# Kernel optimization log

Hardware: AMD Instinct MI355X
Metric: run time of the kernel (lower is better)

Reference implementation:

```python
import jax, jax.numpy as jnp
import numpy as np

B, F, T, EPT, S, E, H, LVL = 16384, 512, 4, 2, 2, 256, 128, 2

def _ple_level(xs_task, x_sh, w_task, b_task, w_sh, b_sh, w_gate, b_gate, w_gsh=None, b_gsh=None):
    # xs_task: [T,B,I] per-task inputs; x_sh: [B,I] shared input
    task_out = jax.nn.relu(jnp.einsum('tbi,teio->tbeo', xs_task, w_task) + b_task[:, None])  # [T,B,EPT,E]
    sh_out = jax.nn.relu(jnp.einsum('bi,sio->bso', x_sh, w_sh) + b_sh)                       # [B,S,E]
    t = task_out.shape[0]
    experts = jnp.concatenate([task_out, jnp.broadcast_to(sh_out[None], (t,) + sh_out.shape)], axis=2)  # [T,B,EPT+S,E]
    gate = jax.nn.softmax(jnp.einsum('tbi,tig->tbg', xs_task, w_gate) + b_gate[:, None], axis=-1)
    task_next = jnp.einsum('tbg,tbge->tbe', gate, experts)  # [T,B,E]
    sh_next = None
    if w_gsh is not None:
        # all experts ordered task0_exp0, task0_exp1, task1_exp0, ..., then shared
        bsz = x_sh.shape[0]
        all_exp = jnp.concatenate([jnp.transpose(task_out, (1, 0, 2, 3)).reshape(bsz, -1, task_out.shape[-1]), sh_out], axis=1)
        gsh = jax.nn.softmax(x_sh @ w_gsh + b_gsh, axis=-1)
        sh_next = jnp.einsum('bg,bge->be', gsh, all_exp)
    return task_next, sh_next

def setup_inputs() -> dict:
    key = jax.random.key(0)
    ks = jax.random.split(key, 16)
    sc = 0.02
    d = {
        'x': jax.random.normal(ks[0], (B, F), jnp.float32),
        # level 0 (in_dim=F, has shared gate)
        'w_task0': jax.random.normal(ks[1], (T, EPT, F, E), jnp.float32) * sc,
        'b_task0': jnp.zeros((T, EPT, E), jnp.float32),
        'w_sh0': jax.random.normal(ks[2], (S, F, E), jnp.float32) * sc,
        'b_sh0': jnp.zeros((S, E), jnp.float32),
        'w_gate0': jax.random.normal(ks[3], (T, F, EPT + S), jnp.float32) * sc,
        'b_gate0': jnp.zeros((T, EPT + S), jnp.float32),
        'w_gsh0': jax.random.normal(ks[4], (F, T * EPT + S), jnp.float32) * sc,
        'b_gsh0': jnp.zeros((T * EPT + S,), jnp.float32),
        # level 1 (last; in_dim=E, no shared gate)
        'w_task1': jax.random.normal(ks[5], (T, EPT, E, E), jnp.float32) * sc,
        'b_task1': jnp.zeros((T, EPT, E), jnp.float32),
        'w_sh1': jax.random.normal(ks[6], (S, E, E), jnp.float32) * sc,
        'b_sh1': jnp.zeros((S, E), jnp.float32),
        'w_gate1': jax.random.normal(ks[7], (T, E, EPT + S), jnp.float32) * sc,
        'b_gate1': jnp.zeros((T, EPT + S), jnp.float32),
        # towers
        'w_tw': jax.random.normal(ks[8], (T, E, H), jnp.float32) * sc,
        'b_tw': jnp.zeros((T, H), jnp.float32),
        'w_out': jax.random.normal(ks[9], (T, H, 2), jnp.float32) * sc,
        'b_out': jnp.zeros((T, 2), jnp.float32),
    }
    return d

def reference(x, w_task0, b_task0, w_sh0, b_sh0, w_gate0, b_gate0, w_gsh0, b_gsh0,
              w_task1, b_task1, w_sh1, b_sh1, w_gate1, b_gate1,
              w_tw, b_tw, w_out, b_out):
    xs_task = jnp.broadcast_to(x[None], (T,) + x.shape)  # all tasks see same input at level 0
    t1, sh1 = _ple_level(xs_task, x, w_task0, b_task0, w_sh0, b_sh0, w_gate0, b_gate0, w_gsh0, b_gsh0)
    t2, _ = _ple_level(t1, sh1, w_task1, b_task1, w_sh1, b_sh1, w_gate1, b_gate1)
    h = jax.nn.relu(jnp.einsum('tbe,teh->tbh', t2, w_tw) + b_tw[:, None])
    logits = jnp.einsum('tbh,tho->tbo', h, w_out) + b_out[:, None]
    p = jax.nn.softmax(logits, axis=-1)
    return jnp.clip(p, 1e-15, 1.0 - 1e-15)  # [T,B,2]
```

## Files before the change

### kernel.cpp

```cpp
#include <hip/hip_runtime.h>

typedef unsigned short u16;
typedef __bf16 bf16x8 __attribute__((ext_vector_type(8)));
typedef float f32x4 __attribute__((ext_vector_type(4)));
typedef u16 u16x8 __attribute__((ext_vector_type(8)));

#define B_ 16384

__device__ __forceinline__ u16 f2b(float f){
  unsigned u = __builtin_bit_cast(unsigned, f);
  u = (u + 0x7FFFu + ((u >> 16) & 1u)) >> 16;
  return (u16)u;
}
__device__ __forceinline__ float b2f(u16 v){
  return __builtin_bit_cast(float, ((unsigned)v) << 16);
}
__device__ __forceinline__ void ld8(const u16* __restrict__ p, float* f){
  u16x8 v = *(const u16x8*)p;
  #pragma unroll
  for (int j = 0; j < 8; ++j) f[j] = b2f(v[j]);
}
__device__ __forceinline__ void st8(u16* __restrict__ p, const float* f){
  u16x8 v;
  #pragma unroll
  for (int j = 0; j < 8; ++j) v[j] = f2b(f[j]);
  *(u16x8*)p = v;
}

__device__ __forceinline__ void gload16(const u16* g, u16* lds){
  __builtin_amdgcn_global_load_lds(
      (const __attribute__((address_space(1))) unsigned int*)g,
      (__attribute__((address_space(3))) unsigned int*)lds, 16, 0, 0);
}

__device__ __forceinline__ void gemm_core(const u16* __restrict__ A,
                                          const u16* __restrict__ Wt,
                                          int K, int m0, int n0,
                                          u16* sA, u16* sB,
                                          f32x4 acc[4][4])
{
  const int tid  = threadIdx.x;
  const int lane = tid & 63;
  const int wave = tid >> 6;
  const int wm   = ((tid >> 7) & 1) * 64;
  const int wn   = ((tid >> 6) & 1) * 64;

  f32x4 zero = {0.f, 0.f, 0.f, 0.f};
  #pragma unroll
  for (int mi = 0; mi < 4; ++mi)
    #pragma unroll
    for (int ni = 0; ni < 4; ++ni)
      acc[mi][ni] = zero;

  const int srow  = lane >> 3;
  const int gslot = (lane & 7) ^ srow;

  const int nsteps = K >> 6;
  for (int ks = 0; ks < nsteps; ++ks) {
    const u16* aB = A  + (size_t)(m0 + wave * 32 + srow) * K + ks * 64 + gslot * 8;
    const u16* bB = Wt + (size_t)(n0 + wave * 32 + srow) * K + ks * 64 + gslot * 8;
    u16* lA = sA + (wave * 4) * 512;
    u16* lB = sB + (wave * 4) * 512;
    #pragma unroll
    for (int i = 0; i < 4; ++i) {
      gload16(aB + (size_t)i * 8 * K, lA + i * 512);
      gload16(bB + (size_t)i * 8 * K, lB + i * 512);
    }
    __syncthreads();
    #pragma unroll
    for (int kk = 0; kk < 2; ++kk) {
      bf16x8 av[4], bv[4];
      #pragma unroll
      for (int mi = 0; mi < 4; ++mi) {
        int r = wm + mi * 16 + (lane & 15);
        int slot = kk * 4 + (lane >> 4);
        av[mi] = *(const bf16x8*)(sA + r * 64 + ((slot ^ (r & 7)) << 3));
      }
      #pragma unroll
      for (int ni = 0; ni < 4; ++ni) {
        int r = wn + ni * 16 + (lane & 15);
        int slot = kk * 4 + (lane >> 4);
        bv[ni] = *(const bf16x8*)(sB + r * 64 + ((slot ^ (r & 7)) << 3));
      }
      #pragma unroll
      for (int mi = 0; mi < 4; ++mi)
        #pragma unroll
        for (int ni = 0; ni < 4; ++ni)
          acc[mi][ni] = __builtin_amdgcn_mfma_f32_16x16x32_bf16(av[mi], bv[ni], acc[mi][ni], 0, 0, 0);
    }
    __syncthreads();
  }
}


__global__ __launch_bounds__(256) void k_gemm0(const u16* __restrict__ xb,
    const u16* __restrict__ Wt0, const float* __restrict__ bias0,
    u16* __restrict__ E0, float* __restrict__ G0L)
{
  __shared__ __align__(16) u16 sm[2 * 128 * 64];
  f32x4 acc[4][4];
  const int bid = blockIdx.x;
  const int swz = (bid & 7) * 336 + (bid >> 3);
  const int m0 = (swz / 21) * 128, n0 = (swz % 21) * 128;
  gemm_core(xb, Wt0, 512, m0, n0, sm, sm + 8192, acc);
  const int lane = threadIdx.x & 63;
  const int wm = ((threadIdx.x >> 7) & 1) * 64, wn = ((threadIdx.x >> 6) & 1) * 64;
  #pragma unroll
  for (int mi = 0; mi < 4; ++mi)
    #pragma unroll
    for (int ni = 0; ni < 4; ++ni) {
      int gcol = n0 + wn + ni * 16 + (lane & 15);
      float bias = bias0[gcol];
      #pragma unroll
      for (int r = 0; r < 4; ++r) {
        int grow = m0 + wm + mi * 16 + ((lane >> 4) << 2) + r;
        float v = acc[mi][ni][r] + bias;
        if (gcol < 2560)      E0[(size_t)grow * 2560 + gcol] = f2b(fmaxf(v, 0.f));
        else if (gcol < 2586) G0L[(size_t)grow * 26 + (gcol - 2560)] = v;
      }
    }
}

__global__ __launch_bounds__(256) void k_mix0(const u16* __restrict__ E0,
    const float* __restrict__ G0L, u16* __restrict__ T1SH)
{
  const int b = blockIdx.x * 8 + (threadIdx.x >> 5);
  const int e0 = (threadIdx.x & 31) * 8;
  const float* gl = G0L + (size_t)b * 26;
  float g[4][4];
  #pragma unroll
  for (int t = 0; t < 4; ++t) {
    float l0 = gl[t*4+0], l1 = gl[t*4+1], l2 = gl[t*4+2], l3 = gl[t*4+3];
    float m = fmaxf(fmaxf(l0, l1), fmaxf(l2, l3));
    float e0e = expf(l0-m), e1 = expf(l1-m), e2 = expf(l2-m), e3 = expf(l3-m);
    float inv = 1.f / (e0e + e1 + e2 + e3);
    g[t][0] = e0e*inv; g[t][1] = e1*inv; g[t][2] = e2*inv; g[t][3] = e3*inv;
  }
  float gs[10];
  {
    float m = gl[16];
    #pragma unroll
    for (int j = 1; j < 10; ++j) m = fmaxf(m, gl[16 + j]);
    float s = 0.f;
    #pragma unroll
    for (int j = 0; j < 10; ++j) { gs[j] = expf(gl[16 + j] - m); s += gs[j]; }
    float inv = 1.f / s;
    #pragma unroll
    for (int j = 0; j < 10; ++j) gs[j] *= inv;
  }
  const u16* row = E0 + (size_t)b * 2560;
  float sh0[8], sh1[8], shacc[8];
  ld8(row + 2048 + e0, sh0);
  ld8(row + 2304 + e0, sh1);
  #pragma unroll
  for (int j = 0; j < 8; ++j) shacc[j] = gs[8]*sh0[j] + gs[9]*sh1[j];
  #pragma unroll
  for (int t = 0; t < 4; ++t) {
    float te0[8], te1[8], v[8];
    ld8(row + (t*2+0)*256 + e0, te0);
    ld8(row + (t*2+1)*256 + e0, te1);
    #pragma unroll
    for (int j = 0; j < 8; ++j) {
      v[j] = g[t][0]*te0[j] + g[t][1]*te1[j] + g[t][2]*sh0[j] + g[t][3]*sh1[j];
      shacc[j] += gs[t*2+0]*te0[j] + gs[t*2+1]*te1[j];
    }
    st8(T1SH + ((size_t)t * B_ + b) * 256 + e0, v);
  }
  st8(T1SH + ((size_t)4 * B_ + b) * 256 + e0, shacc);
}

__global__ __launch_bounds__(256) void k_gemm1(const u16* __restrict__ T1SH,
    const u16* __restrict__ Wt1, const float* __restrict__ bias1,
    u16* __restrict__ E1, float* __restrict__ G1L, u16* __restrict__ SH1E)
{
  const int z = blockIdx.z;
  const int m0 = blockIdx.x * 128, n0 = blockIdx.y * 128;
  if (z == 4 && n0 >= 512) return;
  __shared__ __align__(16) u16 sm[2 * 128 * 64];
  f32x4 acc[4][4];
  gemm_core(T1SH + (size_t)z * B_ * 256, Wt1 + (size_t)z * 640 * 256, 256, m0, n0, sm, sm + 8192, acc);
  const int lane = threadIdx.x & 63;
  const int wm = ((threadIdx.x >> 7) & 1) * 64, wn = ((threadIdx.x >> 6) & 1) * 64;
  const float* bias = bias1 + z * 640;
  #pragma unroll
  for (int mi = 0; mi < 4; ++mi)
    #pragma unroll
    for (int ni = 0; ni < 4; ++ni) {
      int gcol = n0 + wn + ni * 16 + (lane & 15);
      float bv = bias[gcol];
      #pragma unroll
      for (int r = 0; r < 4; ++r) {
        int grow = m0 + wm + mi * 16 + ((lane >> 4) << 2) + r;
        float v = acc[mi][ni][r] + bv;
        if (z < 4) {
          if (gcol < 512)      E1[((size_t)z * B_ + grow) * 512 + gcol] = f2b(fmaxf(v, 0.f));
          else if (gcol < 516) G1L[((size_t)z * B_ + grow) * 4 + (gcol - 512)] = v;
        } else {
          if (gcol < 512)      SH1E[(size_t)grow * 512 + gcol] = f2b(fmaxf(v, 0.f));
        }
      }
    }
}

__global__ __launch_bounds__(256) void k_mix1(const u16* __restrict__ E1,
    const float* __restrict__ G1L, const u16* __restrict__ SH1E, u16* __restrict__ T2)
{
  const int b = blockIdx.x * 8 + (threadIdx.x >> 5);
  const int e0 = (threadIdx.x & 31) * 8;
  float sh0[8], sh1[8];
  ld8(SH1E + (size_t)b * 512 + e0, sh0);
  ld8(SH1E + (size_t)b * 512 + 256 + e0, sh1);
  #pragma unroll
  for (int t = 0; t < 4; ++t) {
    const float* gl = G1L + ((size_t)t * B_ + b) * 4;
    float l0 = gl[0], l1 = gl[1], l2 = gl[2], l3 = gl[3];
    float m = fmaxf(fmaxf(l0, l1), fmaxf(l2, l3));
    float x0 = expf(l0-m), x1 = expf(l1-m), x2 = expf(l2-m), x3 = expf(l3-m);
    float inv = 1.f / (x0 + x1 + x2 + x3);
    float g0 = x0*inv, g1 = x1*inv, g2 = x2*inv, g3 = x3*inv;
    float te0[8], te1[8], v[8];
    ld8(E1 + ((size_t)t * B_ + b) * 512 + e0, te0);
    ld8(E1 + ((size_t)t * B_ + b) * 512 + 256 + e0, te1);
    #pragma unroll
    for (int j = 0; j < 8; ++j)
      v[j] = g0*te0[j] + g1*te1[j] + g2*sh0[j] + g3*sh1[j];
    st8(T2 + ((size_t)t * B_ + b) * 256 + e0, v);
  }
}

__global__ __launch_bounds__(256) void k_tower(const u16* __restrict__ T2,
    const u16* __restrict__ Wtw, const float* __restrict__ b_tw,
    const float* __restrict__ w_out, const float* __restrict__ b_out,
    float* __restrict__ out)
{
  __shared__ __align__(16) u16 sm[2 * 128 * 64];
  __shared__ float part[2][128][2];
  f32x4 acc[4][4];
  const int z = blockIdx.z;
  const int m0 = blockIdx.x * 128;
  gemm_core(T2 + (size_t)z * B_ * 256, Wtw + (size_t)z * 128 * 256, 256, m0, 0, sm, sm + 8192, acc);
  const int lane = threadIdx.x & 63;
  const int wm = ((threadIdx.x >> 7) & 1) * 64, wn = ((threadIdx.x >> 6) & 1) * 64;
  #pragma unroll
  for (int mi = 0; mi < 4; ++mi) {
    #pragma unroll
    for (int r = 0; r < 4; ++r) {
      float p0 = 0.f, p1 = 0.f;
      #pragma unroll
      for (int ni = 0; ni < 4; ++ni) {
        int col = wn + ni * 16 + (lane & 15);
        float h = fmaxf(acc[mi][ni][r] + b_tw[z * 128 + col], 0.f);
        p0 += h * w_out[(z * 128 + col) * 2 + 0];
        p1 += h * w_out[(z * 128 + col) * 2 + 1];
      }
      #pragma unroll
      for (int off = 1; off < 16; off <<= 1) {
        p0 += __shfl_xor(p0, off);
        p1 += __shfl_xor(p1, off);
      }
      if ((lane & 15) == 0) {
        int rowl = wm + mi * 16 + ((lane >> 4) << 2) + r;
        part[wn >> 6][rowl][0] = p0;
        part[wn >> 6][rowl][1] = p1;
      }
    }
  }
  __syncthreads();
  if (threadIdx.x < 128) {
    int rowl = threadIdx.x;
    float l0 = part[0][rowl][0] + part[1][rowl][0] + b_out[z * 2 + 0];
    float l1 = part[0][rowl][1] + part[1][rowl][1] + b_out[z * 2 + 1];
    float mx = fmaxf(l0, l1);
    float e0 = expf(l0 - mx), e1 = expf(l1 - mx);
    float inv = 1.f / (e0 + e1);
    float p0 = fminf(fmaxf(e0 * inv, 1e-15f), 1.0f);
    float p1 = fminf(fmaxf(e1 * inv, 1e-15f), 1.0f);
    size_t o = ((size_t)z * B_ + m0 + rowl) * 2;
    out[o] = p0; out[o + 1] = p1;
  }
}

__global__ void k_prep(const float* __restrict__ x,
    const float* __restrict__ w_task0, const float* __restrict__ b_task0,
    const float* __restrict__ w_sh0,   const float* __restrict__ b_sh0,
    const float* __restrict__ w_gate0, const float* __restrict__ b_gate0,
    const float* __restrict__ w_gsh0,  const float* __restrict__ b_gsh0,
    const float* __restrict__ w_task1, const float* __restrict__ b_task1,
    const float* __restrict__ w_sh1,   const float* __restrict__ b_sh1,
    const float* __restrict__ w_gate1, const float* __restrict__ b_gate1,
    const float* __restrict__ w_tw,
    u16* __restrict__ xb, u16* __restrict__ Wt0, float* __restrict__ bias0,
    u16* __restrict__ Wt1, float* __restrict__ bias1, u16* __restrict__ Wtw)
{
  size_t i = (size_t)blockIdx.x * 256 + threadIdx.x;
  const size_t S_X8  = (size_t)16384 * 512 / 8;
  const size_t S_WT0 = (size_t)2688 * 512;
  const size_t S_B0  = 2688;
  const size_t S_WT1 = (size_t)5 * 640 * 256;
  const size_t S_B1  = 5 * 640;
  const size_t S_WTW = (size_t)4 * 128 * 256;

  if (i < S_X8) {
    size_t o = i * 8;
    float4 a = *(const float4*)(x + o);
    float4 b = *(const float4*)(x + o + 4);
    u16x8 v;
    v[0] = f2b(a.x); v[1] = f2b(a.y); v[2] = f2b(a.z); v[3] = f2b(a.w);
    v[4] = f2b(b.x); v[5] = f2b(b.y); v[6] = f2b(b.z); v[7] = f2b(b.w);
    *(u16x8*)(xb + o) = v;
    return;
  }
  i -= S_X8;
  if (i < S_WT0) {
    int c = (int)(i / 512), f = (int)(i % 512);
    float v = 0.f;
    if (c < 2048)      { int te = c >> 8, o = c & 255; v = w_task0[((size_t)te * 512 + f) * 256 + o]; }
    else if (c < 2560) { int s = (c - 2048) >> 8, o = c & 255; v = w_sh0[((size_t)s * 512 + f) * 256 + o]; }
    else if (c < 2576) { int q = c - 2560; int t = q >> 2, gg = q & 3; v = w_gate0[((size_t)t * 512 + f) * 4 + gg]; }
    else if (c < 2586) { int j = c - 2576; v = w_gsh0[(size_t)f * 10 + j]; }
    Wt0[i] = f2b(v);
    return;
  }
  i -= S_WT0;
  if (i < S_B0) {
    int c = (int)i; float v = 0.f;
    if (c < 2048)      { int te = c >> 8, o = c & 255; v = b_task0[te * 256 + o]; }
    else if (c < 2560) { int s = (c - 2048) >> 8, o = c & 255; v = b_sh0[s * 256 + o]; }
    else if (c < 2576) { v = b_gate0[c - 2560]; }
    else if (c < 2586) { v = b_gsh0[c - 2576]; }
    bias0[c] = v;
    return;
  }
  i -= S_B0;
  if (i < S_WT1) {
    int z = (int)(i / (640 * 256)); int rem = (int)(i % (640 * 256));
    int c = rem / 256, f = rem % 256;
    float v = 0.f;
    if (z < 4) {
      if (c < 512)      { int ee = c >> 8, o = c & 255; v = w_task1[(((size_t)(z * 2 + ee)) * 256 + f) * 256 + o]; }
      else if (c < 516) { int gg = c - 512; v = w_gate1[((size_t)z * 256 + f) * 4 + gg]; }
    } else {
      if (c < 512)      { int s = c >> 8, o = c & 255; v = w_sh1[((size_t)s * 256 + f) * 256 + o]; }
    }
    Wt1[i] = f2b(v);
    return;
  }
  i -= S_WT1;
  if (i < S_B1) {
    int z = (int)(i / 640); int c = (int)(i % 640);
    float v = 0.f;
    if (z < 4) {
      if (c < 512)      { int ee = c >> 8, o = c & 255; v = b_task1[(z * 2 + ee) * 256 + o]; }
      else if (c < 516) { v = b_gate1[z * 4 + (c - 512)]; }
    } else {
      if (c < 512)      { int s = c >> 8, o = c & 255; v = b_sh1[s * 256 + o]; }
    }
    bias1[(size_t)z * 640 + c] = v;
    return;
  }
  i -= S_B1;
  if (i < S_WTW) {
    int z = (int)(i / (128 * 256)); int rem = (int)(i % (128 * 256));
    int h = rem / 256, f = rem % 256;
    Wtw[i] = f2b(w_tw[((size_t)z * 256 + f) * 128 + h]);
    return;
  }
}

extern "C" void kernel_launch(void* const* d_in, const int* in_sizes, int n_in,
                              void* d_out, int out_size, void* d_ws, size_t ws_size,
                              hipStream_t stream)
{
  (void)in_sizes; (void)n_in; (void)out_size; (void)ws_size;
  const float* x       = (const float*)d_in[0];
  const float* w_task0 = (const float*)d_in[1];
  const float* b_task0 = (const float*)d_in[2];
  const float* w_sh0   = (const float*)d_in[3];
  const float* b_sh0   = (const float*)d_in[4];
  const float* w_gate0 = (const float*)d_in[5];
  const float* b_gate0 = (const float*)d_in[6];
  const float* w_gsh0  = (const float*)d_in[7];
  const float* b_gsh0  = (const float*)d_in[8];
  const float* w_task1 = (const float*)d_in[9];
  const float* b_task1 = (const float*)d_in[10];
  const float* w_sh1   = (const float*)d_in[11];
  const float* b_sh1   = (const float*)d_in[12];
  const float* w_gate1 = (const float*)d_in[13];
  const float* b_gate1 = (const float*)d_in[14];
  const float* w_tw    = (const float*)d_in[15];
  const float* b_tw    = (const float*)d_in[16];
  const float* w_out   = (const float*)d_in[17];
  const float* b_out   = (const float*)d_in[18];
  float* out = (float*)d_out;

  char* ws = (char*)d_ws;
  u16*   XB    = (u16*)  (ws + 0);
  u16*   WT0   = (u16*)  (ws + 16777216);
  float* BIAS0 = (float*)(ws + 19529728);
  u16*   WT1   = (u16*)  (ws + 19540480);
  float* BIAS1 = (float*)(ws + 21178880);
  u16*   WTW   = (u16*)  (ws + 21191680);
  u16*   E0    = (u16*)  (ws + 21453824);
  float* G0L   = (float*)(ws + 105339904);
  u16*   T1SH  = (u16*)  (ws + 107043840);
  u16*   E1    = (u16*)  (ws + 148986880);
  float* G1L   = (float*)(ws + 216095744);
  u16*   SH1E  = (u16*)  (ws + 217144320);
  u16*   T2    = (u16*)  (ws + 21453824);

  k_prep<<<13207, 256, 0, stream>>>(x, w_task0, b_task0, w_sh0, b_sh0, w_gate0, b_gate0,
      w_gsh0, b_gsh0, w_task1, b_task1, w_sh1, b_sh1, w_gate1, b_gate1, w_tw,
      XB, WT0, BIAS0, WT1, BIAS1, WTW);
  k_gemm0<<<2688, 256, 0, stream>>>(XB, WT0, BIAS0, E0, G0L);
  k_mix0<<<2048, 256, 0, stream>>>(E0, G0L, T1SH);
  k_gemm1<<<dim3(128, 5, 5), 256, 0, stream>>>(T1SH, WT1, BIAS1, E1, G1L, SH1E);
  k_mix1<<<2048, 256, 0, stream>>>(E1, G1L, SH1E, T2);
  k_tower<<<dim3(128, 1, 4), 256, 0, stream>>>(T2, WTW, b_tw, w_out, b_out, out);
}
```

Measured before the change: 192.7 us.

## Use 256x128 tiles with triple-buffered K=32 LDS pipeline in GEMMs

Replaces the shared GEMM core with a version that uses 512-thread blocks computing 256x128 output tiles, and a 3-stage ring of LDS buffers holding K=32 slices. Global-to-LDS loads are issued two stages ahead, guarded by explicit vmcnt waits and a single barrier per step, so memory latency overlaps with MFMA work and the second barrier per step goes away. The swizzle is adapted to 32-wide rows. All three GEMM kernels and their launch grids and epilogues change to match. The cost is more LDS per block (72 KB), which may reduce occupancy, and the finer K steps mean more barriers overall.

```diff
diff --git a/kernel.cpp b/kernel.cpp
--- a/kernel.cpp
+++ b/kernel.cpp
@@ -6,6 +6,7 @@
 typedef u16 u16x8 __attribute__((ext_vector_type(8)));
 
 #define B_ 16384
+#define XR(r) ((((r) & 3) ^ (((r) >> 2) & 3)))
 
 __device__ __forceinline__ u16 f2b(float f){
   unsigned u = __builtin_bit_cast(unsigned, f);
@@ -33,78 +34,91 @@
       (__attribute__((address_space(3))) unsigned int*)lds, 16, 0, 0);
 }
 
-__device__ __forceinline__ void gemm_core(const u16* __restrict__ A,
-                                          const u16* __restrict__ Wt,
-                                          int K, int m0, int n0,
-                                          u16* sA, u16* sB,
-                                          f32x4 acc[4][4])
+__device__ __forceinline__ void gemm_core2(const u16* __restrict__ A,
+                                           const u16* __restrict__ Wt,
+                                           int K, int m0, int n0, int nt,
+                                           u16* sm, f32x4 acc[4][4])
 {
   const int tid  = threadIdx.x;
   const int lane = tid & 63;
-  const int wave = tid >> 6;
-  const int wm   = ((tid >> 7) & 1) * 64;
+  const int wm   = ((tid >> 7) & 3) * 64;
   const int wn   = ((tid >> 6) & 1) * 64;
 
   f32x4 zero = {0.f, 0.f, 0.f, 0.f};
   #pragma unroll
   for (int mi = 0; mi < 4; ++mi)
     #pragma unroll
-    for (int ni = 0; ni < 4; ++ni)
-      acc[mi][ni] = zero;
-
-  const int srow  = lane >> 3;
-  const int gslot = (lane & 7) ^ srow;
-
-  const int nsteps = K >> 6;
-  for (int ks = 0; ks < nsteps; ++ks) {
-    const u16* aB = A  + (size_t)(m0 + wave * 32 + srow) * K + ks * 64 + gslot * 8;
-    const u16* bB = Wt + (size_t)(n0 + wave * 32 + srow) * K + ks * 64 + gslot * 8;
-    u16* lA = sA + (wave * 4) * 512;
-    u16* lB = sB + (wave * 4) * 512;
-    #pragma unroll
-    for (int i = 0; i < 4; ++i) {
-      gload16(aB + (size_t)i * 8 * K, lA + i * 512);
-      gload16(bB + (size_t)i * 8 * K, lB + i * 512);
-    }
-    __syncthreads();
-    #pragma unroll
-    for (int kk = 0; kk < 2; ++kk) {
-      bf16x8 av[4], bv[4];
+    for (int ni = 0; ni < 4; ++ni) acc[mi][ni] = zero;
+
+  const int rA0 = tid >> 2, rA1 = 128 + (tid >> 2), rB = tid >> 2;
+  const u16* gA0 = A  + (size_t)(m0 + rA0) * K + (((tid & 3) ^ XR(rA0)) * 8);
+  const u16* gA1 = A  + (size_t)(m0 + rA1) * K + (((tid & 3) ^ XR(rA1)) * 8);
+  const u16* gB  = Wt + (size_t)(n0 + rB ) * K + (((tid & 3) ^ XR(rB )) * 8);
+  const int wbase = (tid >> 6) * 512;
+
+  int aoff[4], boff[4];
+  #pragma unroll
+  for (int m = 0; m < 4; ++m) {
+    int r = wm + m * 16 + (lane & 15);
+    aoff[m] = r * 32 + (((lane >> 4) ^ XR(r)) * 8);
+  }
+  #pragma unroll
+  for (int n = 0; n < 4; ++n) {
+    int r = wn + n * 16 + (lane & 15);
+    boff[n] = r * 32 + (((lane >> 4) ^ XR(r)) * 8);
+  }
+
+  #pragma unroll
+  for (int j = 0; j < 2; ++j) {
+    u16* sl = sm + j * 12288;
+    gload16(gA0 + j * 32, sl + wbase);
+    gload16(gA1 + j * 32, sl + 4096 + wbase);
+    gload16(gB  + j * 32, sl + 8192 + wbase);
+  }
+  asm volatile("s_waitcnt vmcnt(3)" ::: "memory");
+  __builtin_amdgcn_s_barrier();
+
+  int cs = 0;
+  for (int j = 0; j < nt; ++j) {
+    if (j + 2 < nt) {
+      int ns = cs + 2; ns = (ns >= 3) ? ns - 3 : ns;
+      u16* sl = sm + ns * 12288;
+      gload16(gA0 + (size_t)(j + 2) * 32, sl + wbase);
+      gload16(gA1 + (size_t)(j + 2) * 32, sl + 4096 + wbase);
+      gload16(gB  + (size_t)(j + 2) * 32, sl + 8192 + wbase);
+    }
+    const u16* sa = sm + cs * 12288;
+    const u16* sb = sa + 8192;
+    bf16x8 av[4], bv[4];
+    #pragma unroll
+    for (int m = 0; m < 4; ++m) av[m] = *(const bf16x8*)(sa + aoff[m]);
+    #pragma unroll
+    for (int n = 0; n < 4; ++n) bv[n] = *(const bf16x8*)(sb + boff[n]);
+    #pragma unroll
+    for (int m = 0; m < 4; ++m)
       #pragma unroll
-      for (int mi = 0; mi < 4; ++mi) {
-        int r = wm + mi * 16 + (lane & 15);
-        int slot = kk * 4 + (lane >> 4);
-        av[mi] = *(const bf16x8*)(sA + r * 64 + ((slot ^ (r & 7)) << 3));
-      }
-      #pragma unroll
-      for (int ni = 0; ni < 4; ++ni) {
-        int r = wn + ni * 16 + (lane & 15);
-        int slot = kk * 4 + (lane >> 4);
-        bv[ni] = *(const bf16x8*)(sB + r * 64 + ((slot ^ (r & 7)) << 3));
-      }
-      #pragma unroll
-      for (int mi = 0; mi < 4; ++mi)
-        #pragma unroll
-        for (int ni = 0; ni < 4; ++ni)
-          acc[mi][ni] = __builtin_amdgcn_mfma_f32_16x16x32_bf16(av[mi], bv[ni], acc[mi][ni], 0, 0, 0);
-    }
-    __syncthreads();
-  }
-}
-
-
-__global__ __launch_bounds__(256) void k_gemm0(const u16* __restrict__ xb,
+      for (int n = 0; n < 4; ++n)
+        acc[m][n] = __builtin_amdgcn_mfma_f32_16x16x32_bf16(av[m], bv[n], acc[m][n], 0, 0, 0);
+    if (j + 2 < nt)      asm volatile("s_waitcnt vmcnt(3)" ::: "memory");
+    else if (j + 1 < nt) asm volatile("s_waitcnt vmcnt(0)" ::: "memory");
+    __builtin_amdgcn_s_barrier();
+    cs = (cs == 2) ? 0 : cs + 1;
+  }
+}
+
+
+__global__ __launch_bounds__(512) void k_gemm0(const u16* __restrict__ xb,
     const u16* __restrict__ Wt0, const float* __restrict__ bias0,
     u16* __restrict__ E0, float* __restrict__ G0L)
 {
-  __shared__ __align__(16) u16 sm[2 * 128 * 64];
+  __shared__ __align__(16) u16 sm[36864];
   f32x4 acc[4][4];
   const int bid = blockIdx.x;
-  const int swz = (bid & 7) * 336 + (bid >> 3);
-  const int m0 = (swz / 21) * 128, n0 = (swz % 21) * 128;
-  gemm_core(xb, Wt0, 512, m0, n0, sm, sm + 8192, acc);
+  const int swz = (bid & 7) * 168 + (bid >> 3);
+  const int m0 = (swz / 21) * 256, n0 = (swz % 21) * 128;
+  gemm_core2(xb, Wt0, 512, m0, n0, 16, sm, acc);
   const int lane = threadIdx.x & 63;
-  const int wm = ((threadIdx.x >> 7) & 1) * 64, wn = ((threadIdx.x >> 6) & 1) * 64;
+  const int wm = ((threadIdx.x >> 7) & 3) * 64, wn = ((threadIdx.x >> 6) & 1) * 64;
   #pragma unroll
   for (int mi = 0; mi < 4; ++mi)
     #pragma unroll
@@ -169,18 +183,18 @@
   st8(T1SH + ((size_t)4 * B_ + b) * 256 + e0, shacc);
 }
 
-__global__ __launch_bounds__(256) void k_gemm1(const u16* __restrict__ T1SH,
+__global__ __launch_bounds__(512) void k_gemm1(const u16* __restrict__ T1SH,
     const u16* __restrict__ Wt1, const float* __restrict__ bias1,
     u16* __restrict__ E1, float* __restrict__ G1L, u16* __restrict__ SH1E)
 {
   const int z = blockIdx.z;
-  const int m0 = blockIdx.x * 128, n0 = blockIdx.y * 128;
+  const int m0 = blockIdx.x * 256, n0 = blockIdx.y * 128;
   if (z == 4 && n0 >= 512) return;
-  __shared__ __align__(16) u16 sm[2 * 128 * 64];
+  __shared__ __align__(16) u16 sm[36864];
   f32x4 acc[4][4];
-  gemm_core(T1SH + (size_t)z * B_ * 256, Wt1 + (size_t)z * 640 * 256, 256, m0, n0, sm, sm + 8192, acc);
+  gemm_core2(T1SH + (size_t)z * B_ * 256, Wt1 + (size_t)z * 640 * 256, 256, m0, n0, 8, sm, acc);
   const int lane = threadIdx.x & 63;
-  const int wm = ((threadIdx.x >> 7) & 1) * 64, wn = ((threadIdx.x >> 6) & 1) * 64;
+  const int wm = ((threadIdx.x >> 7) & 3) * 64, wn = ((threadIdx.x >> 6) & 1) * 64;
   const float* bias = bias1 + z * 640;
   #pragma unroll
   for (int mi = 0; mi < 4; ++mi)
@@ -228,19 +242,19 @@
   }
 }
 
-__global__ __launch_bounds__(256) void k_tower(const u16* __restrict__ T2,
+__global__ __launch_bounds__(512) void k_tower(const u16* __restrict__ T2,
     const u16* __restrict__ Wtw, const float* __restrict__ b_tw,
     const float* __restrict__ w_out, const float* __restrict__ b_out,
     float* __restrict__ out)
 {
-  __shared__ __align__(16) u16 sm[2 * 128 * 64];
-  __shared__ float part[2][128][2];
+  __shared__ __align__(16) u16 sm[36864];
+  __shared__ float part[2][256][2];
   f32x4 acc[4][4];
   const int z = blockIdx.z;
-  const int m0 = blockIdx.x * 128;
-  gemm_core(T2 + (size_t)z * B_ * 256, Wtw + (size_t)z * 128 * 256, 256, m0, 0, sm, sm + 8192, acc);
+  const int m0 = blockIdx.x * 256;
+  gemm_core2(T2 + (size_t)z * B_ * 256, Wtw + (size_t)z * 128 * 256, 256, m0, 0, 8, sm, acc);
   const int lane = threadIdx.x & 63;
-  const int wm = ((threadIdx.x >> 7) & 1) * 64, wn = ((threadIdx.x >> 6) & 1) * 64;
+  const int wm = ((threadIdx.x >> 7) & 3) * 64, wn = ((threadIdx.x >> 6) & 1) * 64;
   #pragma unroll
   for (int mi = 0; mi < 4; ++mi) {
     #pragma unroll
@@ -260,13 +274,13 @@
       }
       if ((lane & 15) == 0) {
         int rowl = wm + mi * 16 + ((lane >> 4) << 2) + r;
-        part[wn >> 6][rowl][0] = p0;
-        part[wn >> 6][rowl][1] = p1;
+        part[(threadIdx.x >> 6) & 1][rowl][0] = p0;
+        part[(threadIdx.x >> 6) & 1][rowl][1] = p1;
       }
     }
   }
   __syncthreads();
-  if (threadIdx.x < 128) {
+  if (threadIdx.x < 256) {
     int rowl = threadIdx.x;
     float l0 = part[0][rowl][0] + part[1][rowl][0] + b_out[z * 2 + 0];
     float l1 = part[0][rowl][1] + part[1][rowl][1] + b_out[z * 2 + 1];
@@ -411,9 +425,9 @@
   k_prep<<<13207, 256, 0, stream>>>(x, w_task0, b_task0, w_sh0, b_sh0, w_gate0, b_gate0,
       w_gsh0, b_gsh0, w_task1, b_task1, w_sh1, b_sh1, w_gate1, b_gate1, w_tw,
       XB, WT0, BIAS0, WT1, BIAS1, WTW);
-  k_gemm0<<<2688, 256, 0, stream>>>(XB, WT0, BIAS0, E0, G0L);
+  k_gemm0<<<1344, 512, 0, stream>>>(XB, WT0, BIAS0, E0, G0L);
   k_mix0<<<2048, 256, 0, stream>>>(E0, G0L, T1SH);
-  k_gemm1<<<dim3(128, 5, 5), 256, 0, stream>>>(T1SH, WT1, BIAS1, E1, G1L, SH1E);
+  k_gemm1<<<dim3(64, 5, 5), 512, 0, stream>>>(T1SH, WT1, BIAS1, E1, G1L, SH1E);
   k_mix1<<<2048, 256, 0, stream>>>(E1, G1L, SH1E, T2);
-  k_tower<<<dim3(128, 1, 4), 256, 0, stream>>>(T2, WTW, b_tw, w_out, b_out, out);
-}
+  k_tower<<<dim3(64, 1, 4), 512, 0, stream>>>(T2, WTW, b_tw, w_out, b_out, out);
+}
```

Result: faster. 181.5 us (-5.8%).

## Double-buffer LDS tiles in GEMM core to overlap global loads with MFMA

Applied to the files above, without the earlier changes.

Replaces the single-buffered GEMM main loop with a double-buffered one: the next K-tile is prefetched into an alternate LDS buffer via global_load_lds while MFMAs run on the current tile, with one wait plus barrier per step instead of two syncthreads. Load source pointers and LDS read offsets are precomputed outside the loop. LDS per block doubles to 64KB, which may lower occupancy, and the extra precomputed addresses raise register pressure.

```diff
diff --git a/kernel.cpp b/kernel.cpp
--- a/kernel.cpp
+++ b/kernel.cpp
@@ -33,11 +33,10 @@
       (__attribute__((address_space(3))) unsigned int*)lds, 16, 0, 0);
 }
 
-__device__ __forceinline__ void gemm_core(const u16* __restrict__ A,
-                                          const u16* __restrict__ Wt,
-                                          int K, int m0, int n0,
-                                          u16* sA, u16* sB,
-                                          f32x4 acc[4][4])
+__device__ __forceinline__ void gemm_core4(const u16* __restrict__ A,
+                                           const u16* __restrict__ Wt,
+                                           int K, int m0, int n0, int nt,
+                                           u16* sm, f32x4 acc[4][4])
 {
   const int tid  = threadIdx.x;
   const int lane = tid & 63;
@@ -49,46 +48,68 @@
   #pragma unroll
   for (int mi = 0; mi < 4; ++mi)
     #pragma unroll
-    for (int ni = 0; ni < 4; ++ni)
-      acc[mi][ni] = zero;
+    for (int ni = 0; ni < 4; ++ni) acc[mi][ni] = zero;
 
   const int srow  = lane >> 3;
   const int gslot = (lane & 7) ^ srow;
-
-  const int nsteps = K >> 6;
-  for (int ks = 0; ks < nsteps; ++ks) {
-    const u16* aB = A  + (size_t)(m0 + wave * 32 + srow) * K + ks * 64 + gslot * 8;
-    const u16* bB = Wt + (size_t)(n0 + wave * 32 + srow) * K + ks * 64 + gslot * 8;
-    u16* lA = sA + (wave * 4) * 512;
-    u16* lB = sB + (wave * 4) * 512;
-    #pragma unroll
-    for (int i = 0; i < 4; ++i) {
-      gload16(aB + (size_t)i * 8 * K, lA + i * 512);
-      gload16(bB + (size_t)i * 8 * K, lB + i * 512);
-    }
-    __syncthreads();
+  const u16* gsrc[8];
+  int gdst[8];
+  #pragma unroll
+  for (int i = 0; i < 8; ++i) {
+    int c = wave * 8 + i;
+    if (c < 16) {
+      gsrc[i] = A + (size_t)(m0 + c * 8 + srow) * K + gslot * 8;
+      gdst[i] = c * 512;
+    } else {
+      gsrc[i] = Wt + (size_t)(n0 + (c - 16) * 8 + srow) * K + gslot * 8;
+      gdst[i] = 8192 + (c - 16) * 512;
+    }
+  }
+
+  int aoff[2][4], boff[2][4];
+  #pragma unroll
+  for (int kk = 0; kk < 2; ++kk) {
+    #pragma unroll
+    for (int m = 0; m < 4; ++m) {
+      int r = wm + m * 16 + (lane & 15);
+      aoff[kk][m] = r * 64 + (((kk * 4 + (lane >> 4)) ^ (r & 7)) * 8);
+    }
+    #pragma unroll
+    for (int n = 0; n < 4; ++n) {
+      int r = wn + n * 16 + (lane & 15);
+      boff[kk][n] = 8192 + r * 64 + (((kk * 4 + (lane >> 4)) ^ (r & 7)) * 8);
+    }
+  }
+
+  #pragma unroll
+  for (int i = 0; i < 8; ++i) gload16(gsrc[i], sm + gdst[i]);
+  asm volatile("s_waitcnt vmcnt(0)" ::: "memory");
+  __builtin_amdgcn_s_barrier();
+
+  for (int j = 0; j < nt; ++j) {
+    if (j + 1 < nt) {
+      u16* base = sm + ((j + 1) & 1) * 16384;
+      #pragma unroll
+      for (int i = 0; i < 8; ++i) gload16(gsrc[i] + (size_t)(j + 1) * 64, base + gdst[i]);
+    }
+    const u16* sa = sm + (j & 1) * 16384;
     #pragma unroll
     for (int kk = 0; kk < 2; ++kk) {
       bf16x8 av[4], bv[4];
       #pragma unroll
-      for (int mi = 0; mi < 4; ++mi) {
-        int r = wm + mi * 16 + (lane & 15);
-        int slot = kk * 4 + (lane >> 4);
-        av[mi] = *(const bf16x8*)(sA + r * 64 + ((slot ^ (r & 7)) << 3));
-      }
-      #pragma unroll
-      for (int ni = 0; ni < 4; ++ni) {
-        int r = wn + ni * 16 + (lane & 15);
-        int slot = kk * 4 + (lane >> 4);
-        bv[ni] = *(const bf16x8*)(sB + r * 64 + ((slot ^ (r & 7)) << 3));
-      }
-      #pragma unroll
-      for (int mi = 0; mi < 4; ++mi)
+      for (int m = 0; m < 4; ++m) av[m] = *(const bf16x8*)(sa + aoff[kk][m]);
+      #pragma unroll
+      for (int n = 0; n < 4; ++n) bv[n] = *(const bf16x8*)(sa + boff[kk][n]);
+      #pragma unroll
+      for (int m = 0; m < 4; ++m)
         #pragma unroll
-        for (int ni = 0; ni < 4; ++ni)
-          acc[mi][ni] = __builtin_amdgcn_mfma_f32_16x16x32_bf16(av[mi], bv[ni], acc[mi][ni], 0, 0, 0);
-    }
-    __syncthreads();
+        for (int n = 0; n < 4; ++n)
+          acc[m][n] = __builtin_amdgcn_mfma_f32_16x16x32_bf16(av[m], bv[n], acc[m][n], 0, 0, 0);
+    }
+    if (j + 1 < nt) {
+      asm volatile("s_waitcnt vmcnt(0)" ::: "memory");
+      __builtin_amdgcn_s_barrier();
+    }
   }
 }
 
@@ -97,12 +118,12 @@
     const u16* __restrict__ Wt0, const float* __restrict__ bias0,
     u16* __restrict__ E0, float* __restrict__ G0L)
 {
-  __shared__ __align__(16) u16 sm[2 * 128 * 64];
+  __shared__ __align__(16) u16 sm[32768];
   f32x4 acc[4][4];
   const int bid = blockIdx.x;
   const int swz = (bid & 7) * 336 + (bid >> 3);
   const int m0 = (swz / 21) * 128, n0 = (swz % 21) * 128;
-  gemm_core(xb, Wt0, 512, m0, n0, sm, sm + 8192, acc);
+  gemm_core4(xb, Wt0, 512, m0, n0, 8, sm, acc);
   const int lane = threadIdx.x & 63;
   const int wm = ((threadIdx.x >> 7) & 1) * 64, wn = ((threadIdx.x >> 6) & 1) * 64;
   #pragma unroll
@@ -176,9 +197,9 @@
   const int z = blockIdx.z;
   const int m0 = blockIdx.x * 128, n0 = blockIdx.y * 128;
   if (z == 4 && n0 >= 512) return;
-  __shared__ __align__(16) u16 sm[2 * 128 * 64];
+  __shared__ __align__(16) u16 sm[32768];
   f32x4 acc[4][4];
-  gemm_core(T1SH + (size_t)z * B_ * 256, Wt1 + (size_t)z * 640 * 256, 256, m0, n0, sm, sm + 8192, acc);
+  gemm_core4(T1SH + (size_t)z * B_ * 256, Wt1 + (size_t)z * 640 * 256, 256, m0, n0, 4, sm, acc);
   const int lane = threadIdx.x & 63;
   const int wm = ((threadIdx.x >> 7) & 1) * 64, wn = ((threadIdx.x >> 6) & 1) * 64;
   const float* bias = bias1 + z * 640;
@@ -233,12 +254,12 @@
     const float* __restrict__ w_out, const float* __restrict__ b_out,
     float* __restrict__ out)
 {
-  __shared__ __align__(16) u16 sm[2 * 128 * 64];
+  __shared__ __align__(16) u16 sm[32768];
   __shared__ float part[2][128][2];
   f32x4 acc[4][4];
   const int z = blockIdx.z;
   const int m0 = blockIdx.x * 128;
-  gemm_core(T2 + (size_t)z * B_ * 256, Wtw + (size_t)z * 128 * 256, 256, m0, 0, sm, sm + 8192, acc);
+  gemm_core4(T2 + (size_t)z * B_ * 256, Wtw + (size_t)z * 128 * 256, 256, m0, 0, 4, sm, acc);
   const int lane = threadIdx.x & 63;
   const int wm = ((threadIdx.x >> 7) & 1) * 64, wn = ((threadIdx.x >> 6) & 1) * 64;
   #pragma unroll
```

Measured after the change: 211.7 us. 1.1x slower.
